# Kernel tuning notes

Measured on AMD Instinct MI355X. Metric: run time of the kernel, lower is better.

The kernel has to match this reference:

```python
import jax, jax.numpy as jnp
import numpy as np
from jax.ops import segment_sum, segment_max, segment_min

N_PER = 128        # nodes (pulses) per graph; graphs are contiguous blocks
NUM_GRAPHS = 2048  # must be a multiple of BATCH_SIZE
K = 4              # knn_graph k (from KNNAmp(4, ...))
BATCH_SIZE = 1024  # hardcoded in the torch module
L1, L2, L3, L4, L5, L6, L7 = 5, 64, 128, 94, 64, 32, 1
GRU_IN = 4 * L5    # 256
GRU_H = L6         # 32


def setup_inputs() -> dict:
    key = jax.random.key(0)
    ks = jax.random.split(key, 12)
    N = N_PER * NUM_GRAPHS
    s = 0.1
    return {
        "x": jax.random.normal(ks[0], (N, L1), jnp.float32),
        "batch": (jnp.arange(N) // N_PER).astype(jnp.int32),
        "h_1": jnp.zeros((2, BATCH_SIZE, GRU_H), jnp.float32),
        "W1": jax.random.normal(ks[1], (2 * L1, L2), jnp.float32) * s,
        "b1": jnp.zeros((L2,), jnp.float32),
        "W2": jax.random.normal(ks[2], (L2, L3), jnp.float32) * s,
        "b2": jnp.zeros((L3,), jnp.float32),
        "nn1_W": jax.random.normal(ks[3], (3 * L3, L4), jnp.float32) * s,
        "nn1_b": jnp.zeros((L4,), jnp.float32),
        "nn2_W": jax.random.normal(ks[4], (L4, L5), jnp.float32) * s,
        "nn2_b": jnp.zeros((L5,), jnp.float32),
        "nn4_W": jax.random.normal(ks[5], (GRU_H, L7), jnp.float32) * s,
        "nn4_b": jnp.zeros((L7,), jnp.float32),
        "wih0": jax.random.normal(ks[6], (3 * GRU_H, GRU_IN), jnp.float32) * s,
        "whh0": jax.random.normal(ks[7], (3 * GRU_H, GRU_H), jnp.float32) * s,
        "bih0": jnp.zeros((3 * GRU_H,), jnp.float32),
        "bhh0": jnp.zeros((3 * GRU_H,), jnp.float32),
        "wih1": jax.random.normal(ks[8], (3 * GRU_H, GRU_H), jnp.float32) * s,
        "whh1": jax.random.normal(ks[9], (3 * GRU_H, GRU_H), jnp.float32) * s,
        "bih1": jnp.zeros((3 * GRU_H,), jnp.float32),
        "bhh1": jnp.zeros((3 * GRU_H,), jnp.float32),
    }


def _knn_neighbors(pos):
    # pos: [N,3]; graphs are contiguous blocks of N_PER nodes -> per-graph KNN
    p = pos.reshape(NUM_GRAPHS, N_PER, 3)
    d2 = jnp.sum((p[:, :, None, :] - p[:, None, :, :]) ** 2, -1)  # [G,n,n]
    d2 = d2 + jnp.eye(N_PER, dtype=d2.dtype) * 1e10               # loop=False
    _, idx = jax.lax.top_k(-d2, K)                                 # [G,n,K]
    off = (jnp.arange(NUM_GRAPHS, dtype=idx.dtype) * N_PER)[:, None, None]
    return (idx + off).reshape(-1, K)  # [N,K] global source (neighbor) ids


def _gru_layer(seq_in, h0, wih, whh, bih, bhh):
    # PyTorch GRU cell math; gate order r, z, n.
    def step(h, xt):
        gi = xt @ wih.T + bih
        gh = h @ whh.T + bhh
        ir, iz, inn = jnp.split(gi, 3, -1)
        hr, hz, hn = jnp.split(gh, 3, -1)
        r = jax.nn.sigmoid(ir + hr)
        z = jax.nn.sigmoid(iz + hz)
        n = jnp.tanh(inn + r * hn)
        hnew = (1.0 - z) * n + z * h
        return hnew, hnew
    hT, ys = jax.lax.scan(step, h0, seq_in)
    return ys, hT


def reference(x, batch, h_1, W1, b1, W2, b2, nn1_W, nn1_b, nn2_W, nn2_b,
              nn4_W, nn4_b, wih0, whh0, bih0, bhh0, wih1, whh1, bih1, bhh1):
    N = x.shape[0]
    nbr = _knn_neighbors(x[:, :3])                       # int indices, non-diff
    x_i = jnp.broadcast_to(x[:, None, :], (N, K, L1))    # center features
    x_j = x[nbr]                                         # [N,K,5] gather
    feats = jnp.concatenate([x_i, x_j - x_i], -1)        # EdgeConv message input
    m = jax.nn.relu(jax.nn.relu(feats @ W1 + b1) @ W2 + b2)  # [N,K,128]
    # three EdgeConvs share the same MLP; compute messages once, aggregate 3 ways
    h = jax.nn.relu(jnp.concatenate([m.max(1), m.mean(1), m.sum(1)], 1))  # [N,384]
    h = jax.nn.relu(h @ nn1_W + nn1_b)
    h = h @ nn2_W + nn2_b                                # [N,64]
    a = segment_max(h, batch, num_segments=NUM_GRAPHS)
    bmin = segment_min(h, batch, num_segments=NUM_GRAPHS)
    c = segment_sum(h, batch, num_segments=NUM_GRAPHS)
    cnt = segment_sum(jnp.ones((N, 1), h.dtype), batch, num_segments=NUM_GRAPHS)
    d = c / cnt
    g = jax.nn.relu(jnp.concatenate([a, bmin, c, d], 1))  # [G,256]
    seq_len = NUM_GRAPHS // BATCH_SIZE
    # faithful to torch.reshape((seq, 256, 1024)).transpose(1,2)
    g = g.reshape(seq_len, GRU_IN, BATCH_SIZE).transpose(0, 2, 1)  # [T,B,256]
    out0, hT0 = _gru_layer(g, h_1[0], wih0, whh0, bih0, bhh0)
    out1, hT1 = _gru_layer(out0, h_1[1], wih1, whh1, bih1, bhh1)
    hT = jnp.stack([hT0, hT1], 0)                        # [2,B,32]
    # torch: reshape(x.transpose(1,2), (-1, 32))
    y = out1.transpose(0, 2, 1).reshape(-1, GRU_H)
    y = jax.nn.relu(y)
    y = jax.nn.relu(y @ nn4_W + nn4_b)                   # [T*B, 1]
    return y, hT
```

## Files before the change

### kernel.cpp

```cpp
#include <hip/hip_runtime.h>
#include <hip/hip_bf16.h>

#define NPER 128

__device__ __forceinline__ void ins4(float d, int id, float* bd, int* bi) {
    const bool c0 = d < bd[0], c1 = d < bd[1], c2 = d < bd[2], c3 = d < bd[3];
    bd[3] = c2 ? bd[2] : (c3 ? d : bd[3]);  bi[3] = c2 ? bi[2] : (c3 ? id : bi[3]);
    bd[2] = c1 ? bd[1] : (c2 ? d : bd[2]);  bi[2] = c1 ? bi[1] : (c2 ? id : bi[2]);
    bd[1] = c0 ? bd[0] : (c1 ? d : bd[1]);  bi[1] = c0 ? bi[0] : (c1 ? id : bi[1]);
    bd[0] = c0 ? d : bd[0];                 bi[0] = c0 ? id : bi[0];
}

__global__ void k_prep(const float* __restrict__ W2,
                       const float* __restrict__ nn2W,
                       const float* __restrict__ nn1W,
                       float* __restrict__ W2I, float* __restrict__ nn2WT,
                       float* __restrict__ WfT)
{
    int i = blockIdx.x * 256 + threadIdx.x;
    if (i < 8192) {
        int ch4 = i >> 8, rem = i & 255, c = rem >> 2, sub = rem & 3;
        W2I[i] = W2[c * 128 + (ch4 * 4 + sub)];
    } else if (i < 8192 + 6016) {
        int j = i - 8192, ch = j / 94, c = j - ch * 94;
        nn2WT[j] = nn2W[c * 64 + ch];
    } else if (i < 8192 + 6016 + 24576) {
        int k = i - 14208, jj = k >> 8, r = k & 255;
        float v = 0.0f;
        if (jj < 94) {
            if (r < 128) v = nn1W[r * 94 + jj];
            else {
                int c = r - 128;
                v = 0.25f * nn1W[(128 + c) * 94 + jj] + nn1W[(256 + c) * 94 + jj];
            }
        }
        WfT[k] = v;
    }
}

__global__ __launch_bounds__(256, 2) void k_edge(
    const float* __restrict__ x,
    const float* __restrict__ W1,
    const float* __restrict__ b1,
    const float* __restrict__ W2I,
    const float* __restrict__ b2,
    const float* __restrict__ WfT,
    const float* __restrict__ nn1b,
    const float* __restrict__ nn2WT,
    const float* __restrict__ nn2b,
    float* __restrict__ pmax,
    float* __restrict__ pmin,
    float* __restrict__ psum)
{
    __shared__ float pool[8192];
    float* XS  = pool;
    float* KD  = pool + 640;
    int*   KI  = (int*)(pool + 1664);
    int*   NBR = (int*)(pool + 2688);
    float* AGM = pool;
    float* AGS = pool + 4096;
    float* NNH = pool;
    float* HT  = pool;

    const int t = threadIdx.x;
    const int lane = t & 63;
    const int w = __builtin_amdgcn_readfirstlane(t >> 6);
    const int graph = blockIdx.x >> 1;
    const int node0 = (blockIdx.x & 1) * 64;

    for (int i = t; i < NPER * 5; i += 256) XS[i] = x[(size_t)graph * (NPER * 5) + i];
    __syncthreads();

    {
        const int nl2 = t & 63;
        const int q  = t >> 6;
        const int ng2 = node0 + nl2;
        const float px = XS[ng2 * 5 + 0], py = XS[ng2 * 5 + 1], pz = XS[ng2 * 5 + 2];
        float bd[4] = {3e38f, 3e38f, 3e38f, 3e38f};
        int   bi[4] = {0, 0, 0, 0};
        const int m0 = q * 32;
        for (int m = m0; m < m0 + 32; ++m) {
            float dx = XS[m * 5 + 0] - px, dy = XS[m * 5 + 1] - py, dz = XS[m * 5 + 2] - pz;
            float d2 = __fadd_rn(__fadd_rn(__fmul_rn(dx, dx), __fmul_rn(dy, dy)),
                                 __fmul_rn(dz, dz));
            d2 = (m == ng2) ? 3.0e38f : d2;
            ins4(d2, m, bd, bi);
        }
        #pragma unroll
        for (int s = 0; s < 4; ++s) { KD[(q * 4 + s) * 64 + nl2] = bd[s]; KI[(q * 4 + s) * 64 + nl2] = bi[s]; }
    }
    __syncthreads();
    if (t < 64) {
        float bd[4] = {3e38f, 3e38f, 3e38f, 3e38f};
        int   bi[4] = {0, 0, 0, 0};
        #pragma unroll
        for (int q = 0; q < 4; ++q)
            #pragma unroll
            for (int s = 0; s < 4; ++s)
                ins4(KD[(q * 4 + s) * 64 + t], KI[(q * 4 + s) * 64 + t], bd, bi);
        #pragma unroll
        for (int s = 0; s < 4; ++s) NBR[t * 4 + s] = bi[s];
    }
    __syncthreads();

    const int nl = t >> 2;
    const int kk = t & 3;
    const int n_g = node0 + nl;
    const int j   = NBR[nl * 4 + kk];
    float f[10];
    #pragma unroll
    for (int d = 0; d < 5; ++d) { f[d] = XS[n_g * 5 + d]; f[5 + d] = XS[j * 5 + d] - f[d]; }
    float h1v[64];
    #pragma unroll
    for (int c = 0; c < 64; ++c) h1v[c] = b1[c];
    #pragma unroll
    for (int d = 0; d < 10; ++d) {
        float fd = f[d];
        #pragma unroll
        for (int c = 0; c < 64; ++c) h1v[c] = fmaf(fd, W1[d * 64 + c], h1v[c]);
    }
    #pragma unroll
    for (int c = 0; c < 64; ++c) h1v[c] = fmaxf(h1v[c], 0.0f);
    __syncthreads();

    float acc[24];
    const int jj0 = __builtin_amdgcn_readfirstlane(w * 24);
    #pragma unroll
    for (int i = 0; i < 24; ++i) acc[i] = (jj0 + i < 94) ? nn1b[jj0 + i] : 0.0f;

    for (int h = 0; h < 2; ++h) {
        for (int ch = 0; ch < 64; ch += 4) {
            const float* wp = W2I + (size_t)(h * 16 + (ch >> 2)) * 256;
            float m0 = b2[h * 64 + ch], m1 = b2[h * 64 + ch + 1];
            float m2 = b2[h * 64 + ch + 2], m3 = b2[h * 64 + ch + 3];
            #pragma unroll
            for (int c = 0; c < 64; ++c) {
                float hv = h1v[c];
                m0 = fmaf(hv, wp[c * 4 + 0], m0);
                m1 = fmaf(hv, wp[c * 4 + 1], m1);
                m2 = fmaf(hv, wp[c * 4 + 2], m2);
                m3 = fmaf(hv, wp[c * 4 + 3], m3);
            }
            m0 = fmaxf(m0, 0.0f); m1 = fmaxf(m1, 0.0f);
            m2 = fmaxf(m2, 0.0f); m3 = fmaxf(m3, 0.0f);
            float x0 = fmaxf(m0, __shfl_xor(m0, 1));
            float x1 = fmaxf(m1, __shfl_xor(m1, 1));
            float x2 = fmaxf(m2, __shfl_xor(m2, 1));
            float x3 = fmaxf(m3, __shfl_xor(m3, 1));
            x0 = fmaxf(x0, __shfl_xor(x0, 2));
            x1 = fmaxf(x1, __shfl_xor(x1, 2));
            x2 = fmaxf(x2, __shfl_xor(x2, 2));
            x3 = fmaxf(x3, __shfl_xor(x3, 2));
            float s0 = m0 + __shfl_xor(m0, 1);
            float s1 = m1 + __shfl_xor(m1, 1);
            float s2 = m2 + __shfl_xor(m2, 1);
            float s3 = m3 + __shfl_xor(m3, 1);
            s0 += __shfl_xor(s0, 2);
            s1 += __shfl_xor(s1, 2);
            s2 += __shfl_xor(s2, 2);
            s3 += __shfl_xor(s3, 2);
            if (kk == 0) {
                const int sw = (((ch >> 2) ^ nl) & 15) << 2;
                *(float4*)&AGM[(nl << 6) + sw] = make_float4(x0, x1, x2, x3);
                *(float4*)&AGS[(nl << 6) + sw] = make_float4(s0, s1, s2, s3);
            }
        }
        __syncthreads();

        for (int cb = 0; cb < 64; cb += 8) {
            float am[8], as_[8];
            #pragma unroll
            for (int i = 0; i < 2; ++i) {
                const int sw = ((((cb >> 2) + i) ^ lane) & 15) << 2;
                *(float4*)&am[i * 4]  = *(const float4*)&AGM[(lane << 6) + sw];
                *(float4*)&as_[i * 4] = *(const float4*)&AGS[(lane << 6) + sw];
            }
            #pragma unroll
            for (int i2 = 0; i2 < 24; ++i2) {
                const float* wa = WfT + (size_t)(jj0 + i2) * 256 + h * 64 + cb;
                const float* wb = wa + 128;
                float a = acc[i2];
                #pragma unroll
                for (int i = 0; i < 8; ++i) a = fmaf(am[i], wa[i], fmaf(as_[i], wb[i], a));
                acc[i2] = a;
            }
        }
        __syncthreads();
    }

    #pragma unroll
    for (int i2 = 0; i2 < 24; ++i2)
        if (jj0 + i2 < 94) NNH[(jj0 + i2) * 64 + lane] = fmaxf(acc[i2], 0.0f);
    __syncthreads();

    {
        const int ch0 = __builtin_amdgcn_readfirstlane(w * 16);
        float acc2[16];
        #pragma unroll
        for (int i = 0; i < 16; ++i) acc2[i] = nn2b[ch0 + i];
        #pragma unroll 1
        for (int cb = 0; cb < 64; cb += 32) {
            float hv[32];
            #pragma unroll
            for (int i = 0; i < 32; ++i) hv[i] = NNH[(cb + i) * 64 + lane];
            #pragma unroll
            for (int i = 0; i < 16; ++i) {
                const float* wp = nn2WT + (size_t)(ch0 + i) * 94 + cb;
                float a = acc2[i];
                #pragma unroll
                for (int c = 0; c < 32; ++c) a = fmaf(hv[c], wp[c], a);
                acc2[i] = a;
            }
        }
        {
            float hv[30];
            #pragma unroll
            for (int i = 0; i < 30; ++i) hv[i] = NNH[(64 + i) * 64 + lane];
            #pragma unroll
            for (int i = 0; i < 16; ++i) {
                const float* wp = nn2WT + (size_t)(ch0 + i) * 94 + 64;
                float a = acc2[i];
                #pragma unroll
                for (int c = 0; c < 30; ++c) a = fmaf(hv[c], wp[c], a);
                acc2[i] = a;
            }
        }
        __syncthreads();
        #pragma unroll
        for (int i = 0; i < 8; ++i)
            *(float2*)&HT[lane * 66 + ch0 + i * 2] =
                make_float2(acc2[i * 2], acc2[i * 2 + 1]);
    }
    __syncthreads();

    if (t < 64) {
        float mx = -3e38f, mn = 3e38f, sm = 0.0f;
        for (int n = 0; n < 64; ++n) {
            float v = HT[n * 66 + t];
            mx = fmaxf(mx, v); mn = fminf(mn, v); sm += v;
        }
        pmax[(size_t)blockIdx.x * 64 + t] = mx;
        pmin[(size_t)blockIdx.x * 64 + t] = mn;
        psum[(size_t)blockIdx.x * 64 + t] = sm;
    }
}

__global__ void k_pool(const float* __restrict__ pmax, const float* __restrict__ pmin,
                       const float* __restrict__ psum, float* __restrict__ g_out)
{
    const int t = threadIdx.x;
    const int g = blockIdx.x * 4 + (t >> 6);
    const int ch = t & 63;
    const size_t a = (size_t)(2 * g) * 64 + ch, b = a + 64;
    float mx = fmaxf(pmax[a], pmax[b]);
    float mn = fminf(pmin[a], pmin[b]);
    float sm = psum[a] + psum[b];
    float* gp = g_out + (size_t)g * 256;
    gp[ch]        = fmaxf(mx, 0.0f);
    gp[64 + ch]   = fmaxf(mn, 0.0f);
    gp[128 + ch]  = fmaxf(sm, 0.0f);
    gp[192 + ch]  = fmaxf(sm * (1.0f / 128.0f), 0.0f);
}

__global__ __launch_bounds__(128) void k_gru(
    const float* __restrict__ g, const float* __restrict__ h1_in,
    const float* __restrict__ wih0, const float* __restrict__ whh0,
    const float* __restrict__ bih0, const float* __restrict__ bhh0,
    const float* __restrict__ wih1, const float* __restrict__ whh1,
    const float* __restrict__ bih1, const float* __restrict__ bhh1,
    float* __restrict__ out1, float* __restrict__ hT)
{
    __shared__ float xt[4][256];
    __shared__ float h0[4][32];
    __shared__ float h1l[4][32];
    const int tid = threadIdx.x;
    const int e = tid >> 5;
    const int j = tid & 31;
    const int b = blockIdx.x * 4 + e;

    h0[e][j]  = h1_in[b * 32 + j];
    h1l[e][j] = h1_in[32768 + b * 32 + j];
    __syncthreads();

    for (int t = 0; t < 2; ++t) {
        for (int c = j; c < 256; c += 32)
            xt[e][c] = g[(size_t)(t * 1024 + 4 * c + (b >> 8)) * 256 + (b & 255)];
        __syncthreads();

        float gi0 = bih0[j], gi1 = bih0[32 + j], gi2 = bih0[64 + j];
        for (int c = 0; c < 256; ++c) {
            float xv = xt[e][c];
            gi0 += xv * wih0[j * 256 + c];
            gi1 += xv * wih0[(32 + j) * 256 + c];
            gi2 += xv * wih0[(64 + j) * 256 + c];
        }
        float gh0 = bhh0[j], gh1 = bhh0[32 + j], gh2 = bhh0[64 + j];
        #pragma unroll
        for (int c = 0; c < 32; ++c) {
            float hv = h0[e][c];
            gh0 += hv * whh0[j * 32 + c];
            gh1 += hv * whh0[(32 + j) * 32 + c];
            gh2 += hv * whh0[(64 + j) * 32 + c];
        }
        float r = 1.0f / (1.0f + expf(-(gi0 + gh0)));
        float z = 1.0f / (1.0f + expf(-(gi1 + gh1)));
        float nn = tanhf(gi2 + r * gh2);
        float hn0 = (1.0f - z) * nn + z * h0[e][j];
        __syncthreads();
        h0[e][j] = hn0;
        __syncthreads();

        float ai0 = bih1[j], ai1 = bih1[32 + j], ai2 = bih1[64 + j];
        #pragma unroll
        for (int c = 0; c < 32; ++c) {
            float xv = h0[e][c];
            ai0 += xv * wih1[j * 32 + c];
            ai1 += xv * wih1[(32 + j) * 32 + c];
            ai2 += xv * wih1[(64 + j) * 32 + c];
        }
        float ah0 = bhh1[j], ah1 = bhh1[32 + j], ah2 = bhh1[64 + j];
        #pragma unroll
        for (int c = 0; c < 32; ++c) {
            float hv = h1l[e][c];
            ah0 += hv * whh1[j * 32 + c];
            ah1 += hv * whh1[(32 + j) * 32 + c];
            ah2 += hv * whh1[(64 + j) * 32 + c];
        }
        float r1 = 1.0f / (1.0f + expf(-(ai0 + ah0)));
        float z1 = 1.0f / (1.0f + expf(-(ai1 + ah1)));
        float n1 = tanhf(ai2 + r1 * ah2);
        float hn1 = (1.0f - z1) * n1 + z1 * h1l[e][j];
        __syncthreads();
        h1l[e][j] = hn1;
        out1[(size_t)(t * 1024 + b) * 32 + j] = hn1;
        __syncthreads();
    }
    hT[b * 32 + j]         = h0[e][j];
    hT[32768 + b * 32 + j] = h1l[e][j];
}

__global__ void k_final(const float* __restrict__ out1,
                        const float* __restrict__ nn4W, const float* __restrict__ nn4b,
                        float* __restrict__ y)
{
    const int r = blockIdx.x * 256 + threadIdx.x;
    if (r >= 2048) return;
    const int t = r >> 10, rp = r & 1023;
    const int f = rp >> 5, bb0 = (rp & 31) << 5;
    float acc = nn4b[0];
    #pragma unroll
    for (int c = 0; c < 32; ++c)
        acc += fmaxf(out1[(size_t)(t * 1024 + bb0 + c) * 32 + f], 0.0f) * nn4W[c];
    y[r] = fmaxf(acc, 0.0f);
}

extern "C" void kernel_launch(void* const* d_in, const int* in_sizes, int n_in,
                              void* d_out, int out_size, void* d_ws, size_t ws_size,
                              hipStream_t stream) {
    const float* x    = (const float*)d_in[0];
    const float* h1i  = (const float*)d_in[2];
    const float* W1   = (const float*)d_in[3];
    const float* b1   = (const float*)d_in[4];
    const float* W2   = (const float*)d_in[5];
    const float* b2   = (const float*)d_in[6];
    const float* nn1W = (const float*)d_in[7];
    const float* nn1b = (const float*)d_in[8];
    const float* nn2W = (const float*)d_in[9];
    const float* nn2b = (const float*)d_in[10];
    const float* nn4W = (const float*)d_in[11];
    const float* nn4b = (const float*)d_in[12];
    const float* wih0 = (const float*)d_in[13];
    const float* whh0 = (const float*)d_in[14];
    const float* bih0 = (const float*)d_in[15];
    const float* bhh0 = (const float*)d_in[16];
    const float* wih1 = (const float*)d_in[17];
    const float* whh1 = (const float*)d_in[18];
    const float* bih1 = (const float*)d_in[19];
    const float* bhh1 = (const float*)d_in[20];

    float* ws = (float*)d_ws;
    float* g_buf  = ws;
    float* out1   = g_buf + 524288;
    float* W2I    = out1 + 65536;
    float* nn2WT  = W2I + 8192;
    float* WfT    = nn2WT + 6016;
    float* pmax   = WfT + 24576;
    float* pmin   = pmax + 262144;
    float* psum   = pmin + 262144;

    float* y  = (float*)d_out;
    float* hT = y + 2048;

    hipLaunchKernelGGL(k_prep, dim3(152), dim3(256), 0, stream,
                       W2, nn2W, nn1W, W2I, nn2WT, WfT);
    hipLaunchKernelGGL(k_edge, dim3(4096), dim3(256), 0, stream,
                       x, W1, b1, W2I, b2, WfT, nn1b, nn2WT, nn2b,
                       pmax, pmin, psum);
    hipLaunchKernelGGL(k_pool, dim3(512), dim3(256), 0, stream,
                       pmax, pmin, psum, g_buf);
    hipLaunchKernelGGL(k_gru, dim3(256), dim3(128), 0, stream,
                       g_buf, h1i, wih0, whh0, bih0, bhh0,
                       wih1, whh1, bih1, bhh1, out1, hT);
    hipLaunchKernelGGL(k_final, dim3(8), dim3(256), 0, stream,
                       out1, nn4W, nn4b, y);
}
```

Baseline: 896.3 us.

## Compute second edge MLP layer with split-bf16 MFMA instead of scalar FMAs

Replaces the per-edge scalar 64x128 FP32 matmul in k_edge with bf16 MFMA 16x16x32. Precision is kept close to FP32 by splitting both activations and W2 into hi/lo bf16 parts and issuing three MFMAs (hi*hi, hi*lo, lo*hi). W2 is pre-swizzled into MFMA B-operand layout in k_prep. Activations are staged through LDS in two halves, and max/sum over the K neighbours is reduced in registers from the MFMA accumulator layout. Launch bounds move to 3 blocks per CU and LDS use grows, which adds register and LDS pressure and some rounding deviation.

```diff
diff --git a/kernel.cpp b/kernel.cpp
--- a/kernel.cpp
+++ b/kernel.cpp
@@ -2,6 +2,18 @@
 #include <hip/hip_bf16.h>
 
 #define NPER 128
+
+typedef __attribute__((ext_vector_type(8))) short s8v;
+typedef __attribute__((ext_vector_type(4))) float f4v;
+
+__device__ __forceinline__ unsigned short f2bf(float x) {
+    unsigned u = __float_as_uint(x);
+    unsigned r = u + 0x7FFFu + ((u >> 16) & 1u);
+    return (unsigned short)(r >> 16);
+}
+__device__ __forceinline__ float bf2f(unsigned short b) {
+    return __uint_as_float(((unsigned)b) << 16);
+}
 
 __device__ __forceinline__ void ins4(float d, int id, float* bd, int* bi) {
     const bool c0 = d < bd[0], c1 = d < bd[1], c2 = d < bd[2], c3 = d < bd[3];
@@ -14,18 +26,16 @@
 __global__ void k_prep(const float* __restrict__ W2,
                        const float* __restrict__ nn2W,
                        const float* __restrict__ nn1W,
-                       float* __restrict__ W2I, float* __restrict__ nn2WT,
-                       float* __restrict__ WfT)
+                       float* __restrict__ nn2WT, float* __restrict__ WfT,
+                       unsigned short* __restrict__ WBhi,
+                       unsigned short* __restrict__ WBlo)
 {
     int i = blockIdx.x * 256 + threadIdx.x;
-    if (i < 8192) {
-        int ch4 = i >> 8, rem = i & 255, c = rem >> 2, sub = rem & 3;
-        W2I[i] = W2[c * 128 + (ch4 * 4 + sub)];
-    } else if (i < 8192 + 6016) {
-        int j = i - 8192, ch = j / 94, c = j - ch * 94;
-        nn2WT[j] = nn2W[c * 64 + ch];
-    } else if (i < 8192 + 6016 + 24576) {
-        int k = i - 14208, jj = k >> 8, r = k & 255;
+    if (i < 6016) {
+        int ch = i / 94, c = i - ch * 94;
+        nn2WT[i] = nn2W[c * 64 + ch];
+    } else if (i < 30592) {
+        int k = i - 6016, jj = k >> 8, r = k & 255;
         float v = 0.0f;
         if (jj < 94) {
             if (r < 128) v = nn1W[r * 94 + jj];
@@ -35,15 +45,25 @@
             }
         }
         WfT[k] = v;
-    }
-}
-
-__global__ __launch_bounds__(256, 2) void k_edge(
+    } else if (i < 38784) {
+        int j = i - 30592;
+        int e = j & 7, l = (j >> 3) & 63, nt = (j >> 9) & 7, ks = j >> 12;
+        int kk = ks * 32 + ((l >> 4) << 3) + e;
+        int n  = nt * 16 + (l & 15);
+        float v = W2[kk * 128 + n];
+        unsigned short hb = f2bf(v);
+        WBhi[j] = hb;
+        WBlo[j] = f2bf(v - bf2f(hb));
+    }
+}
+
+__global__ __launch_bounds__(256, 3) void k_edge(
     const float* __restrict__ x,
     const float* __restrict__ W1,
     const float* __restrict__ b1,
-    const float* __restrict__ W2I,
     const float* __restrict__ b2,
+    const unsigned short* __restrict__ WBhi,
+    const unsigned short* __restrict__ WBlo,
     const float* __restrict__ WfT,
     const float* __restrict__ nn1b,
     const float* __restrict__ nn2WT,
@@ -52,15 +72,17 @@
     float* __restrict__ pmin,
     float* __restrict__ psum)
 {
-    __shared__ float pool[8192];
+    __shared__ float pool[10240];
     float* XS  = pool;
-    float* KD  = pool + 640;
-    int*   KI  = (int*)(pool + 1664);
-    int*   NBR = (int*)(pool + 2688);
-    float* AGM = pool;
-    float* AGS = pool + 4096;
+    int*   NBR = (int*)(pool + 640);
+    float* KD  = pool + 896;
+    int*   KI  = (int*)(pool + 1920);
+    unsigned short* PH16 = (unsigned short*)(pool + 1024);
+    unsigned short* PL16 = (unsigned short*)(pool + 5632);
+    float* AGM = pool + 1024;
+    float* AGS = pool + 5120;
     float* NNH = pool;
-    float* HT  = pool;
+    float* HT  = pool + 6016;
 
     const int t = threadIdx.x;
     const int lane = t & 63;
@@ -121,50 +143,101 @@
     }
     #pragma unroll
     for (int c = 0; c < 64; ++c) h1v[c] = fmaxf(h1v[c], 0.0f);
-    __syncthreads();
+
+    float mxs[2][2][8], sms[2][2][8];
+    #pragma unroll
+    for (int c = 0; c < 2; ++c) {
+        if ((t >> 7) == c) {
+            const int rl = t & 127;
+            unsigned int* dh = (unsigned int*)PH16 + rl * 36;
+            unsigned int* dl = (unsigned int*)PL16 + rl * 36;
+            #pragma unroll
+            for (int i = 0; i < 8; ++i) {
+                unsigned int hw[4], lw[4];
+                #pragma unroll
+                for (int p = 0; p < 4; ++p) {
+                    float va = h1v[i * 8 + p * 2], vb = h1v[i * 8 + p * 2 + 1];
+                    unsigned short ha = f2bf(va), hb = f2bf(vb);
+                    unsigned short la = f2bf(va - bf2f(ha)), lb = f2bf(vb - bf2f(hb));
+                    hw[p] = (unsigned)ha | ((unsigned)hb << 16);
+                    lw[p] = (unsigned)la | ((unsigned)lb << 16);
+                }
+                *(uint4*)(dh + 4 * i) = make_uint4(hw[0], hw[1], hw[2], hw[3]);
+                *(uint4*)(dl + 4 * i) = make_uint4(lw[0], lw[1], lw[2], lw[3]);
+            }
+        }
+        __syncthreads();
+
+        #pragma unroll
+        for (int hf = 0; hf < 2; ++hf) {
+            f4v C[2][4];
+            #pragma unroll
+            for (int q = 0; q < 4; ++q) {
+                float bv = b2[hf * 64 + q * 16 + (lane & 15)];
+                #pragma unroll
+                for (int m = 0; m < 2; ++m) {
+                    C[m][q][0] = bv; C[m][q][1] = bv; C[m][q][2] = bv; C[m][q][3] = bv;
+                }
+            }
+            #pragma unroll
+            for (int ks = 0; ks < 2; ++ks) {
+                s8v ah[2], al[2];
+                #pragma unroll
+                for (int m = 0; m < 2; ++m) {
+                    const int row = (w << 5) + (m << 4) + (lane & 15);
+                    const int ui  = row * 72 + (ks << 5) + ((lane >> 4) << 3);
+                    ah[m] = *(const s8v*)(PH16 + ui);
+                    al[m] = *(const s8v*)(PL16 + ui);
+                }
+                #pragma unroll
+                for (int q = 0; q < 4; ++q) {
+                    const int nt = hf * 4 + q;
+                    const int bidx = ((((ks << 3) | nt) << 6) | lane) << 3;
+                    s8v bh = *(const s8v*)(WBhi + bidx);
+                    s8v bl = *(const s8v*)(WBlo + bidx);
+                    #pragma unroll
+                    for (int m = 0; m < 2; ++m) {
+                        f4v cc = C[m][q];
+                        cc = __builtin_amdgcn_mfma_f32_16x16x32_bf16(al[m], bh, cc, 0, 0, 0);
+                        cc = __builtin_amdgcn_mfma_f32_16x16x32_bf16(ah[m], bl, cc, 0, 0, 0);
+                        cc = __builtin_amdgcn_mfma_f32_16x16x32_bf16(ah[m], bh, cc, 0, 0, 0);
+                        C[m][q] = cc;
+                    }
+                }
+            }
+            #pragma unroll
+            for (int m = 0; m < 2; ++m)
+                #pragma unroll
+                for (int q = 0; q < 4; ++q) {
+                    float a0 = fmaxf(C[m][q][0], 0.0f), a1 = fmaxf(C[m][q][1], 0.0f);
+                    float a2 = fmaxf(C[m][q][2], 0.0f), a3 = fmaxf(C[m][q][3], 0.0f);
+                    mxs[c][m][hf * 4 + q] = fmaxf(fmaxf(a0, a1), fmaxf(a2, a3));
+                    sms[c][m][hf * 4 + q] = (a0 + a1) + (a2 + a3);
+                }
+        }
+        __syncthreads();
+    }
 
     float acc[24];
     const int jj0 = __builtin_amdgcn_readfirstlane(w * 24);
     #pragma unroll
     for (int i = 0; i < 24; ++i) acc[i] = (jj0 + i < 94) ? nn1b[jj0 + i] : 0.0f;
 
+    #pragma unroll
     for (int h = 0; h < 2; ++h) {
-        for (int ch = 0; ch < 64; ch += 4) {
-            const float* wp = W2I + (size_t)(h * 16 + (ch >> 2)) * 256;
-            float m0 = b2[h * 64 + ch], m1 = b2[h * 64 + ch + 1];
-            float m2 = b2[h * 64 + ch + 2], m3 = b2[h * 64 + ch + 3];
-            #pragma unroll
-            for (int c = 0; c < 64; ++c) {
-                float hv = h1v[c];
-                m0 = fmaf(hv, wp[c * 4 + 0], m0);
-                m1 = fmaf(hv, wp[c * 4 + 1], m1);
-                m2 = fmaf(hv, wp[c * 4 + 2], m2);
-                m3 = fmaf(hv, wp[c * 4 + 3], m3);
-            }
-            m0 = fmaxf(m0, 0.0f); m1 = fmaxf(m1, 0.0f);
-            m2 = fmaxf(m2, 0.0f); m3 = fmaxf(m3, 0.0f);
-            float x0 = fmaxf(m0, __shfl_xor(m0, 1));
-            float x1 = fmaxf(m1, __shfl_xor(m1, 1));
-            float x2 = fmaxf(m2, __shfl_xor(m2, 1));
-            float x3 = fmaxf(m3, __shfl_xor(m3, 1));
-            x0 = fmaxf(x0, __shfl_xor(x0, 2));
-            x1 = fmaxf(x1, __shfl_xor(x1, 2));
-            x2 = fmaxf(x2, __shfl_xor(x2, 2));
-            x3 = fmaxf(x3, __shfl_xor(x3, 2));
-            float s0 = m0 + __shfl_xor(m0, 1);
-            float s1 = m1 + __shfl_xor(m1, 1);
-            float s2 = m2 + __shfl_xor(m2, 1);
-            float s3 = m3 + __shfl_xor(m3, 1);
-            s0 += __shfl_xor(s0, 2);
-            s1 += __shfl_xor(s1, 2);
-            s2 += __shfl_xor(s2, 2);
-            s3 += __shfl_xor(s3, 2);
-            if (kk == 0) {
-                const int sw = (((ch >> 2) ^ nl) & 15) << 2;
-                *(float4*)&AGM[(nl << 6) + sw] = make_float4(x0, x1, x2, x3);
-                *(float4*)&AGS[(nl << 6) + sw] = make_float4(s0, s1, s2, s3);
-            }
-        }
+        #pragma unroll
+        for (int c2 = 0; c2 < 2; ++c2)
+            #pragma unroll
+            for (int m = 0; m < 2; ++m)
+                #pragma unroll
+                for (int q = 0; q < 4; ++q) {
+                    const int nt   = h * 4 + q;
+                    const int node = (c2 << 5) + (w << 3) + (m << 2) + (lane >> 4);
+                    const int chl  = (q << 4) + (lane & 15);
+                    const int ad   = (node << 6) + ((((chl >> 2) ^ node) & 15) << 2) + (chl & 3);
+                    AGM[ad] = mxs[c2][m][nt];
+                    AGS[ad] = sms[c2][m][nt];
+                }
         __syncthreads();
 
         for (int cb = 0; cb < 64; cb += 8) {
@@ -381,20 +454,21 @@
     float* ws = (float*)d_ws;
     float* g_buf  = ws;
     float* out1   = g_buf + 524288;
-    float* W2I    = out1 + 65536;
-    float* nn2WT  = W2I + 8192;
+    float* nn2WT  = out1 + 65536;
     float* WfT    = nn2WT + 6016;
     float* pmax   = WfT + 24576;
     float* pmin   = pmax + 262144;
     float* psum   = pmin + 262144;
+    unsigned short* WBhi = (unsigned short*)(psum + 262144);
+    unsigned short* WBlo = WBhi + 8192;
 
     float* y  = (float*)d_out;
     float* hT = y + 2048;
 
     hipLaunchKernelGGL(k_prep, dim3(152), dim3(256), 0, stream,
-                       W2, nn2W, nn1W, W2I, nn2WT, WfT);
+                       W2, nn2W, nn1W, nn2WT, WfT, WBhi, WBlo);
     hipLaunchKernelGGL(k_edge, dim3(4096), dim3(256), 0, stream,
-                       x, W1, b1, W2I, b2, WfT, nn1b, nn2WT, nn2b,
+                       x, W1, b1, b2, WBhi, WBlo, WfT, nn1b, nn2WT, nn2b,
                        pmax, pmin, psum);
     hipLaunchKernelGGL(k_pool, dim3(512), dim3(256), 0, stream,
                        pmax, pmin, psum, g_buf);
```

Result: faster. 823.4 us (-8.1%).
